# Performance work log

Hardware: AMD Instinct MI355X
Metric: run time of the kernel (lower is better)

The kernel has to match this reference:

```python
import jax, jax.numpy as jnp
import numpy as np

B, S, D = 4, 2048, 1024
H, DK, DV, DOUT = 16, 64, 64, 1024
NEG = -1.0e9


def setup_inputs() -> dict:
    key = jax.random.key(0)
    ks = jax.random.split(key, 12)
    sq = lambda fan_in: 1.0 / np.sqrt(fan_in)
    return {
        "query": jax.random.normal(ks[0], (B, S, D), jnp.float32),
        "key": jax.random.normal(ks[1], (B, S, D), jnp.float32),
        "value": jax.random.normal(ks[2], (B, S, D), jnp.float32),
        "attention_mask": jax.random.randint(ks[3], (B, 1, 1, S), 0, 2, jnp.int32),
        "wq": jax.random.normal(ks[4], (D, H * DK), jnp.float32) * sq(D),
        "bq": jnp.zeros((H * DK,), jnp.float32),
        "wk": jax.random.normal(ks[5], (D, H * DK), jnp.float32) * sq(D),
        "bk": jnp.zeros((H * DK,), jnp.float32),
        "wv": jax.random.normal(ks[6], (D, H * DV), jnp.float32) * sq(D),
        "bv": jnp.zeros((H * DV,), jnp.float32),
        "wo": jax.random.normal(ks[7], (H * DV, DOUT), jnp.float32) * sq(H * DV),
        "bo": jnp.zeros((DOUT,), jnp.float32),
    }


def _split_heads(x, head_dim):
    b, s, _ = x.shape
    return x.reshape(b, s, H, head_dim).transpose(0, 2, 1, 3)  # [B,H,S,hd]


def reference(query, key, value, attention_mask, wq, bq, wk, bk, wv, bv, wo, bo):
    q = _split_heads(query @ wq + bq, DK)   # [B,H,S,DK]
    k = _split_heads(key @ wk + bk, DK)     # [B,H,S,DK]
    v = _split_heads(value @ wv + bv, DV)   # [B,H,S,DV]
    logits = jnp.einsum("bhqd,bhkd->bhqk", q, k) / jnp.sqrt(jnp.float32(DK))
    logits = logits + attention_mask.astype(logits.dtype) * NEG
    attn = jax.nn.softmax(logits, axis=-1)
    out = jnp.einsum("bhqk,bhkd->bhqd", attn, v)          # [B,H,S,DV]
    out = out.transpose(0, 2, 1, 3).reshape(query.shape[0], -1, H * DV)
    return out @ wo + bo
```

## Files before the change

### kernel.cpp

```cpp
#include <hip/hip_runtime.h>
#include <hip/hip_bf16.h>
#include <math.h>

#define Bv 4
#define Sv 2048
#define Dv 1024
#define Hv 16
#define HD 64
#define NEGV (-1.0e9f)

typedef __attribute__((ext_vector_type(8))) short bf16x8;
typedef __attribute__((ext_vector_type(4))) short s16x4;
typedef __attribute__((ext_vector_type(4))) float f32x4;

__device__ __forceinline__ short f2bf(float f) {
    union { __hip_bfloat16 h; short s; } u;
    u.h = __float2bfloat16(f);
    return u.s;
}

#if __has_builtin(__builtin_amdgcn_exp2f)
#define EXP2F(x) __builtin_amdgcn_exp2f(x)
#else
#define EXP2F(x) __expf((x) * 0.6931471805599453f)
#endif

__device__ __forceinline__ void glds16(const void* g, void* l) {
    __builtin_amdgcn_global_load_lds(
        (const __attribute__((address_space(1))) void*)g,
        (__attribute__((address_space(3))) void*)l, 16, 0, 0);
}

__global__ __launch_bounds__(256) void cvt_bf16(const float* __restrict__ X,
                                                unsigned short* __restrict__ Y) {
    const size_t i = ((size_t)blockIdx.x * 256 + threadIdx.x) * 8;
    const float4 a = *(const float4*)&X[i];
    const float4 b = *(const float4*)&X[i + 4];
    bf16x8 o = {f2bf(a.x), f2bf(a.y), f2bf(a.z), f2bf(a.w),
                f2bf(b.x), f2bf(b.y), f2bf(b.z), f2bf(b.w)};
    *(bf16x8*)&Y[i] = o;
}

__device__ __forceinline__ void transpose_w_body(const float* __restrict__ W,
                                                 unsigned short* __restrict__ WT) {
    __shared__ float T[64][65];
    const int t = threadIdx.x;
    const int n0 = blockIdx.x * 64, k0 = blockIdx.y * 64;
    #pragma unroll
    for (int i = 0; i < 4; ++i) {
        const int k = (t >> 4) + 16 * i;
        const int nc = (t & 15) * 4;
        const float4 v = *(const float4*)&W[(size_t)(k0 + k) * 1024 + n0 + nc];
        T[k][nc + 0] = v.x; T[k][nc + 1] = v.y;
        T[k][nc + 2] = v.z; T[k][nc + 3] = v.w;
    }
    __syncthreads();
    const int n = t >> 2, kc = (t & 3) * 16;
    #pragma unroll
    for (int j4 = 0; j4 < 4; ++j4) {
        s16x4 o;
        #pragma unroll
        for (int jj = 0; jj < 4; ++jj) o[jj] = f2bf(T[kc + j4 * 4 + jj][n]);
        *(s16x4*)&WT[(size_t)(n0 + n) * 1024 + k0 + kc + j4 * 4] = o;
    }
}

__global__ __launch_bounds__(256) void transpose_w(const float* __restrict__ W,
                                                   unsigned short* __restrict__ WT) {
    transpose_w_body(W, WT);
}

__global__ __launch_bounds__(256) void transpose_w4(const float* __restrict__ W0,
                                                    const float* __restrict__ W1,
                                                    const float* __restrict__ W2,
                                                    const float* __restrict__ W3,
                                                    unsigned short* __restrict__ WTb) {
    const int z = blockIdx.z;
    const float* W = (z == 0) ? W0 : (z == 1) ? W1 : (z == 2) ? W2 : W3;
    transpose_w_body(W, WTb + (size_t)z * 1048576);
}

__global__ __launch_bounds__(256) void transpose_v(const unsigned short* __restrict__ Vin,
                                                   unsigned short* __restrict__ VT) {
    __shared__ unsigned short T[64][72];
    const int t = threadIdx.x;
    const int s0 = blockIdx.x * 64;
    const int bh = blockIdx.y;
    const size_t ib = (size_t)bh * Sv * 64;
    const size_t ob = (size_t)bh * 64 * Sv;
    {
        const int s = t >> 2, dc = (t & 3) * 16;
        const bf16x8 a = *(const bf16x8*)&Vin[ib + (size_t)(s0 + s) * 64 + dc];
        const bf16x8 b = *(const bf16x8*)&Vin[ib + (size_t)(s0 + s) * 64 + dc + 8];
        *(bf16x8*)&T[s][dc] = a;
        *(bf16x8*)&T[s][dc + 8] = b;
    }
    __syncthreads();
    const int dv = t >> 2, sc = (t & 3) * 16;
    #pragma unroll
    for (int j4 = 0; j4 < 4; ++j4) {
        s16x4 o;
        #pragma unroll
        for (int jj = 0; jj < 4; ++jj) o[jj] = (short)T[sc + j4 * 4 + jj][dv];
        *(s16x4*)&VT[ob + (size_t)dv * Sv + s0 + sc + j4 * 4] = o;
    }
}

template <int PERM>
__global__ __launch_bounds__(256) void gemm_mfma(const unsigned short* __restrict__ X,
                                                 const unsigned short* __restrict__ WT,
                                                 const float* __restrict__ bias,
                                                 void* __restrict__ Cv,
                                                 int M, int N, int K) {
    __shared__ short As[128 * 32];
    __shared__ short Bs[128 * 32];

    const int t = threadIdx.x;
    const int lane = t & 63, w = t >> 6;
    const int l15 = lane & 15, quad = lane >> 4;
    const int m0 = blockIdx.y * 128, n0 = blockIdx.x * 128;
    const int wm = (w >> 1) * 64, wn = (w & 1) * 64;

    f32x4 acc[4][4];
    #pragma unroll
    for (int mi = 0; mi < 4; ++mi)
        #pragma unroll
        for (int ni = 0; ni < 4; ++ni) acc[mi][ni] = (f32x4){0.f, 0.f, 0.f, 0.f};

    const int srow = lane >> 2;
    const int skc = (lane & 3) * 8;

    for (int k0 = 0; k0 < K; k0 += 32) {
        #pragma unroll
        for (int i = 0; i < 2; ++i) {
            const int seg = w * 2 + i;
            const int row = seg * 16 + srow;
            glds16(&WT[(size_t)(n0 + row) * K + k0 + skc], &Bs[seg * 512]);
            glds16(&X[(size_t)(m0 + row) * K + k0 + skc], &As[seg * 512]);
        }
        __syncthreads();

        bf16x8 afr[4], bfr[4];
        #pragma unroll
        for (int mi = 0; mi < 4; ++mi)
            afr[mi] = *(const bf16x8*)&As[(wm + mi * 16 + l15) * 32 + quad * 8];
        #pragma unroll
        for (int ni = 0; ni < 4; ++ni)
            bfr[ni] = *(const bf16x8*)&Bs[(wn + ni * 16 + l15) * 32 + quad * 8];
        #pragma unroll
        for (int mi = 0; mi < 4; ++mi)
            #pragma unroll
            for (int ni = 0; ni < 4; ++ni)
                acc[mi][ni] = __builtin_amdgcn_mfma_f32_16x16x32_bf16(
                    afr[mi], bfr[ni], acc[mi][ni], 0, 0, 0);
        __syncthreads();
    }

    #pragma unroll
    for (int mi = 0; mi < 4; ++mi) {
        #pragma unroll
        for (int ni = 0; ni < 4; ++ni) {
            const int col = n0 + wn + ni * 16 + l15;
            const float bsv = bias[col];
            #pragma unroll
            for (int r = 0; r < 4; ++r) {
                const int row = m0 + wm + mi * 16 + quad * 4 + r;
                const float vv = acc[mi][ni][r] + bsv;
                if constexpr (PERM == 0) {
                    ((float*)Cv)[(size_t)row * N + col] = vv;
                } else {
                    const int bb = row / Sv, s = row % Sv;
                    const int hh = col >> 6, d = col & 63;
                    ((unsigned short*)Cv)[((((size_t)bb * Hv + hh) * Sv + s) << 6) + d] =
                        (unsigned short)f2bf(vv);
                }
            }
        }
    }
}

__global__ __launch_bounds__(256) void gemm_qkv(const float* __restrict__ Xq,
                                                const float* __restrict__ Xk,
                                                const float* __restrict__ Xv,
                                                const unsigned short* __restrict__ WTb,
                                                const float* __restrict__ bq,
                                                const float* __restrict__ bk,
                                                const float* __restrict__ bv,
                                                unsigned short* __restrict__ Oq,
                                                unsigned short* __restrict__ Ok,
                                                unsigned short* __restrict__ Ov) {
    __shared__ short As[128 * 32];
    __shared__ short Bs[128 * 32];

    const int hw = blockIdx.x + 8 * (blockIdx.y + 64 * blockIdx.z);
    const int wl = (hw & 7) * 192 + (hw >> 3);
    const int bx = wl & 7, by = (wl >> 3) & 63, bz = wl >> 9;

    const float* X = (bz == 0) ? Xq : (bz == 1) ? Xk : Xv;
    const unsigned short* WT = WTb + (size_t)bz * 1048576;
    const float* bias = (bz == 0) ? bq : (bz == 1) ? bk : bv;

    const int t = threadIdx.x;
    const int lane = t & 63, w = t >> 6;
    const int l15 = lane & 15, quad = lane >> 4;
    const int m0 = by * 128, n0 = bx * 128;
    const int wm = (w >> 1) * 64, wn = (w & 1) * 64;

    f32x4 acc[4][4];
    #pragma unroll
    for (int mi = 0; mi < 4; ++mi)
        #pragma unroll
        for (int ni = 0; ni < 4; ++ni) acc[mi][ni] = (f32x4){0.f, 0.f, 0.f, 0.f};

    const int srow = lane >> 2;
    const int skc = (lane & 3) * 8;

    for (int k0 = 0; k0 < 1024; k0 += 32) {
        float4 fa[2][2];
        #pragma unroll
        for (int i = 0; i < 2; ++i) {
            const int seg = w * 2 + i;
            const int row = seg * 16 + srow;
            glds16(&WT[(size_t)(n0 + row) * 1024 + k0 + skc], &Bs[seg * 512]);
            const float* src = &X[(size_t)(m0 + row) * 1024 + k0 + skc];
            fa[i][0] = *(const float4*)src;
            fa[i][1] = *(const float4*)(src + 4);
        }
        #pragma unroll
        for (int i = 0; i < 2; ++i) {
            const int seg = w * 2 + i;
            bf16x8 o = {f2bf(fa[i][0].x), f2bf(fa[i][0].y), f2bf(fa[i][0].z), f2bf(fa[i][0].w),
                        f2bf(fa[i][1].x), f2bf(fa[i][1].y), f2bf(fa[i][1].z), f2bf(fa[i][1].w)};
            *(bf16x8*)&As[seg * 512 + lane * 8] = o;
        }
        __syncthreads();

        bf16x8 afr[4], bfr[4];
        #pragma unroll
        for (int mi = 0; mi < 4; ++mi)
            afr[mi] = *(const bf16x8*)&As[(wm + mi * 16 + l15) * 32 + quad * 8];
        #pragma unroll
        for (int ni = 0; ni < 4; ++ni)
            bfr[ni] = *(const bf16x8*)&Bs[(wn + ni * 16 + l15) * 32 + quad * 8];
        #pragma unroll
        for (int mi = 0; mi < 4; ++mi)
            #pragma unroll
            for (int ni = 0; ni < 4; ++ni)
                acc[mi][ni] = __builtin_amdgcn_mfma_f32_16x16x32_bf16(
                    afr[mi], bfr[ni], acc[mi][ni], 0, 0, 0);
        __syncthreads();
    }

    #pragma unroll
    for (int mi = 0; mi < 4; ++mi) {
        #pragma unroll
        for (int ni = 0; ni < 4; ++ni) {
            const int col = n0 + wn + ni * 16 + l15;
            const float bsv = bias[col];
            const int hh = col >> 6, d = col & 63;
            #pragma unroll
            for (int r = 0; r < 4; ++r) {
                const int row = m0 + wm + mi * 16 + quad * 4 + r;
                const int bb = row >> 11, s = row & 2047;
                const unsigned short v = (unsigned short)f2bf(acc[mi][ni][r] + bsv);
                if (bz == 2) {
                    Ov[((((size_t)bb * Hv + hh) * 64 + d) << 11) + s] = v;
                } else {
                    unsigned short* O = (bz == 0) ? Oq : Ok;
                    O[((((size_t)bb * Hv + hh) * Sv + s) << 6) + d] = v;
                }
            }
        }
    }
}

__global__ __launch_bounds__(256) void gemm_out(const unsigned short* __restrict__ Xp,
                                                const unsigned short* __restrict__ WT,
                                                const float* __restrict__ bias,
                                                float* __restrict__ C) {
    __shared__ short As[128 * 32];
    __shared__ short Bs[128 * 32];

    const int hw = blockIdx.x + 8 * blockIdx.y;
    const int wl = (hw & 7) * 64 + (hw >> 3);
    const int bx = wl & 7, by = wl >> 3;

    const int t = threadIdx.x;
    const int lane = t & 63, w = t >> 6;
    const int l15 = lane & 15, quad = lane >> 4;
    const int m0 = by * 128, n0 = bx * 128;
    const int wm = (w >> 1) * 64, wn = (w & 1) * 64;

    f32x4 acc[4][4];
    #pragma unroll
    for (int mi = 0; mi < 4; ++mi)
        #pragma unroll
        for (int ni = 0; ni < 4; ++ni) acc[mi][ni] = (f32x4){0.f, 0.f, 0.f, 0.f};

    const int srow = lane >> 2;
    const int skc = (lane & 3) * 8;

    for (int k0 = 0; k0 < 1024; k0 += 32) {
        const int hh = k0 >> 6, db = (k0 & 63);
        #pragma unroll
        for (int i = 0; i < 2; ++i) {
            const int seg = w * 2 + i;
            const int row = seg * 16 + srow;
            glds16(&WT[(size_t)(n0 + row) * 1024 + k0 + skc], &Bs[seg * 512]);
            const int rb = m0 + row;
            const int bb = rb >> 11, s = rb & 2047;
            glds16(&Xp[((((size_t)bb * Hv + hh) * Sv + s) << 6) + db + skc], &As[seg * 512]);
        }
        __syncthreads();

        bf16x8 afr[4], bfr[4];
        #pragma unroll
        for (int mi = 0; mi < 4; ++mi)
            afr[mi] = *(const bf16x8*)&As[(wm + mi * 16 + l15) * 32 + quad * 8];
        #pragma unroll
        for (int ni = 0; ni < 4; ++ni)
            bfr[ni] = *(const bf16x8*)&Bs[(wn + ni * 16 + l15) * 32 + quad * 8];
        #pragma unroll
        for (int mi = 0; mi < 4; ++mi)
            #pragma unroll
            for (int ni = 0; ni < 4; ++ni)
                acc[mi][ni] = __builtin_amdgcn_mfma_f32_16x16x32_bf16(
                    afr[mi], bfr[ni], acc[mi][ni], 0, 0, 0);
        __syncthreads();
    }

    #pragma unroll
    for (int mi = 0; mi < 4; ++mi) {
        #pragma unroll
        for (int ni = 0; ni < 4; ++ni) {
            const int col = n0 + wn + ni * 16 + l15;
            const float bsv = bias[col];
            #pragma unroll
            for (int r = 0; r < 4; ++r) {
                const int row = m0 + wm + mi * 16 + quad * 4 + r;
                C[(size_t)row * 1024 + col] = acc[mi][ni][r] + bsv;
            }
        }
    }
}

template <int OL>
__global__ __launch_bounds__(256, 4) void attn_mfma(const unsigned short* __restrict__ Q,
                                                    const unsigned short* __restrict__ Kg,
                                                    const unsigned short* __restrict__ VT,
                                                    const int* __restrict__ mask,
                                                    unsigned short* __restrict__ O) {
    __shared__ short Kl[64 * 72];
    __shared__ short Vl[64 * 72];
    __shared__ short Sl[128 * 72];
    __shared__ float Mk[64];

    const int t = threadIdx.x;
    const int lane = t & 63, w = t >> 6;
    const int l15 = lane & 15, quad = lane >> 4;
    const int q0 = blockIdx.x * 128;
    const int h = blockIdx.y, b = blockIdx.z;
    const int bh = b * Hv + h;
    const size_t kvb = (size_t)bh * Sv * 64;
    const size_t vtb = (size_t)bh * 64 * Sv;

    bf16x8 qf[2][2];
    #pragma unroll
    for (int ni = 0; ni < 2; ++ni) {
        const size_t qa = kvb + (size_t)(q0 + w * 32 + ni * 16 + l15) * 64 + quad * 8;
        qf[ni][0] = *(const bf16x8*)&Q[qa];
        qf[ni][1] = *(const bf16x8*)&Q[qa + 32];
    }

    float l_acc[2] = {0.f, 0.f};
    f32x4 oacc[2][4];
    #pragma unroll
    for (int mi = 0; mi < 2; ++mi)
        #pragma unroll
        for (int ni = 0; ni < 4; ++ni) oacc[mi][ni] = (f32x4){0.f, 0.f, 0.f, 0.f};

    const int srow = t >> 2, sch = (t & 3) * 16;
    const unsigned short* Kst = Kg + kvb + (size_t)srow * 64 + sch;
    const unsigned short* Vst = VT + vtb + (size_t)srow * Sv + sch;
    const int* Mst = mask + (size_t)b * Sv;

    bf16x8 kr0 = *(const bf16x8*)&Kst[0];
    bf16x8 kr1 = *(const bf16x8*)&Kst[8];
    bf16x8 vr0 = *(const bf16x8*)&Vst[0];
    bf16x8 vr1 = *(const bf16x8*)&Vst[8];
    int mreg = (t < 64) ? Mst[t] : 0;

    constexpr float CS = 0.18033688011112042f;
    constexpr float CM = NEGV * 1.4426950408889634f;

    for (int k0 = 0; k0 < Sv; k0 += 64) {
        __syncthreads();
        *(bf16x8*)&Kl[srow * 72 + sch] = kr0;
        *(bf16x8*)&Kl[srow * 72 + sch + 8] = kr1;
        *(bf16x8*)&Vl[srow * 72 + sch] = vr0;
        *(bf16x8*)&Vl[srow * 72 + sch + 8] = vr1;
        if (t < 64) Mk[t] = CM * (float)mreg;
        __syncthreads();

        if (k0 + 64 < Sv) {
            kr0 = *(const bf16x8*)&Kst[(size_t)(k0 + 64) * 64];
            kr1 = *(const bf16x8*)&Kst[(size_t)(k0 + 64) * 64 + 8];
            vr0 = *(const bf16x8*)&Vst[k0 + 64];
            vr1 = *(const bf16x8*)&Vst[k0 + 64 + 8];
            if (t < 64) mreg = Mst[k0 + 64 + t];
        }

        #pragma unroll
        for (int mi = 0; mi < 4; ++mi) {
            const bf16x8 kf0 = *(const bf16x8*)&Kl[(mi * 16 + l15) * 72 + quad * 8];
            const bf16x8 kf1 = *(const bf16x8*)&Kl[(mi * 16 + l15) * 72 + 32 + quad * 8];
            const float4 mk4 = *(const float4*)&Mk[mi * 16 + quad * 4];
            #pragma unroll
            for (int ni = 0; ni < 2; ++ni) {
                f32x4 st = (f32x4){0.f, 0.f, 0.f, 0.f};
                st = __builtin_amdgcn_mfma_f32_16x16x32_bf16(kf0, qf[ni][0], st, 0, 0, 0);
                st = __builtin_amdgcn_mfma_f32_16x16x32_bf16(kf1, qf[ni][1], st, 0, 0, 0);
                const float p0 = EXP2F(__builtin_fmaf(st[0], CS, mk4.x));
                const float p1 = EXP2F(__builtin_fmaf(st[1], CS, mk4.y));
                const float p2 = EXP2F(__builtin_fmaf(st[2], CS, mk4.z));
                const float p3 = EXP2F(__builtin_fmaf(st[3], CS, mk4.w));
                l_acc[ni] += (p0 + p1) + (p2 + p3);
                s16x4 pv = {f2bf(p0), f2bf(p1), f2bf(p2), f2bf(p3)};
                *(s16x4*)&Sl[(w * 32 + ni * 16 + l15) * 72 + mi * 16 + quad * 4] = pv;
            }
        }

        bf16x8 vf[4][2];
        #pragma unroll
        for (int ni = 0; ni < 4; ++ni) {
            vf[ni][0] = *(const bf16x8*)&Vl[(ni * 16 + l15) * 72 + quad * 8];
            vf[ni][1] = *(const bf16x8*)&Vl[(ni * 16 + l15) * 72 + 32 + quad * 8];
        }

        #pragma unroll
        for (int mi = 0; mi < 2; ++mi) {
            const bf16x8 pf0 = *(const bf16x8*)&Sl[(w * 32 + mi * 16 + l15) * 72 + quad * 8];
            const bf16x8 pf1 = *(const bf16x8*)&Sl[(w * 32 + mi * 16 + l15) * 72 + 32 + quad * 8];
            #pragma unroll
            for (int ni = 0; ni < 4; ++ni) {
                oacc[mi][ni] = __builtin_amdgcn_mfma_f32_16x16x32_bf16(pf0, vf[ni][0], oacc[mi][ni], 0, 0, 0);
                oacc[mi][ni] = __builtin_amdgcn_mfma_f32_16x16x32_bf16(pf1, vf[ni][1], oacc[mi][ni], 0, 0, 0);
            }
        }
    }

    #pragma unroll
    for (int mi = 0; mi < 2; ++mi) {
        float l = l_acc[mi];
        l += __shfl_xor(l, 16);
        l += __shfl_xor(l, 32);
        #pragma unroll
        for (int r = 0; r < 4; ++r) {
            const float lr = __shfl(l, quad * 4 + r, 64);
            const float inv = 1.0f / lr;
            const int s = q0 + w * 32 + mi * 16 + quad * 4 + r;
            #pragma unroll
            for (int ni = 0; ni < 4; ++ni) {
                const unsigned short v = (unsigned short)f2bf(oacc[mi][ni][r] * inv);
                if constexpr (OL == 0) {
                    O[((size_t)b * Sv + s) * (Hv * HD) + h * HD + ni * 16 + l15] = v;
                } else {
                    O[kvb + ((size_t)s << 6) + ni * 16 + l15] = v;
                }
            }
        }
    }
}

extern "C" void kernel_launch(void* const* d_in, const int* in_sizes, int n_in,
                              void* d_out, int out_size, void* d_ws, size_t ws_size,
                              hipStream_t stream) {
    const float* query = (const float*)d_in[0];
    const float* key   = (const float*)d_in[1];
    const float* value = (const float*)d_in[2];
    const int*   amask = (const int*)d_in[3];
    const float* wq = (const float*)d_in[4];
    const float* bq = (const float*)d_in[5];
    const float* wk = (const float*)d_in[6];
    const float* bk = (const float*)d_in[7];
    const float* wv = (const float*)d_in[8];
    const float* bv = (const float*)d_in[9];
    const float* wo = (const float*)d_in[10];
    const float* bo = (const float*)d_in[11];
    float* out = (float*)d_out;

    unsigned short* wsp = (unsigned short*)d_ws;
    dim3 bb(256);

    if (ws_size >= (size_t)64 * 1024 * 1024) {
        const size_t PBQ = (size_t)Bv * Hv * Sv * HD;
        unsigned short* qb = wsp;
        unsigned short* kb = qb + PBQ;
        unsigned short* vb = kb + PBQ;
        unsigned short* ab = vb + PBQ;

        transpose_w4<<<dim3(16, 16, 4), bb, 0, stream>>>(wq, wk, wv, wo, ab);

        gemm_qkv<<<dim3(8, 64, 3), bb, 0, stream>>>(query, key, value, ab,
                                                    bq, bk, bv, qb, kb, vb);

        attn_mfma<1><<<dim3(Sv / 128, Hv, Bv), bb, 0, stream>>>(qb, kb, vb, amask, qb);

        gemm_out<<<dim3(8, 64), bb, 0, stream>>>(qb, ab + (size_t)3 * 1048576, bo, out);
    } else {
        const size_t PQ = (size_t)Hv * Sv * HD;
        unsigned short* qb = wsp;
        unsigned short* kb = qb + PQ;
        unsigned short* vb = kb + PQ;
        unsigned short* ab = vb + PQ;
        const int M = Sv;
        dim3 gg(8, M / 128), gc(M * 1024 / 2048), gt(16, 16);
        for (int b = 0; b < Bv; ++b) {
            const size_t xoff = (size_t)b * Sv * Dv;
            unsigned short* wt_kb = kb;
            unsigned short* wt_out = (unsigned short*)(out + xoff);
            unsigned short* wt_vb = vb;

            cvt_bf16<<<gc, bb, 0, stream>>>(value + xoff, ab);
            transpose_w<<<gt, bb, 0, stream>>>(wv, wt_kb);
            gemm_mfma<1><<<gg, bb, 0, stream>>>(ab, wt_kb, bv, qb, M, 1024, 1024);
            transpose_v<<<dim3(Sv / 64, Hv), bb, 0, stream>>>(qb, vb);

            cvt_bf16<<<gc, bb, 0, stream>>>(query + xoff, ab);
            transpose_w<<<gt, bb, 0, stream>>>(wq, wt_kb);
            gemm_mfma<1><<<gg, bb, 0, stream>>>(ab, wt_kb, bq, qb, M, 1024, 1024);

            cvt_bf16<<<gc, bb, 0, stream>>>(key + xoff, ab);
            transpose_w<<<gt, bb, 0, stream>>>(wk, wt_out);
            gemm_mfma<1><<<gg, bb, 0, stream>>>(ab, wt_out, bk, kb, M, 1024, 1024);

            attn_mfma<0><<<dim3(Sv / 128, Hv, 1), bb, 0, stream>>>(qb, kb, vb,
                                                                   amask + (size_t)b * Sv, ab);

            transpose_w<<<gt, bb, 0, stream>>>(wo, wt_vb);
            gemm_mfma<0><<<gg, bb, 0, stream>>>(ab, wt_vb, bo, out + xoff, M, 1024, 1024);
        }
    }
}
```

Before: 394.3 us.

## Pre-convert QKV inputs to bf16 and load GEMM A tiles via global_load_lds

Adds a cvt3 kernel that converts query/key/value from fp32 to bf16 in a separate pass. The QKV projection GEMM then loads its A tiles directly into LDS with global_load_lds instead of loading fp32 into registers and converting in the inner loop. The aim is to cut register pressure and per-iteration conversion work and halve the A-operand bytes the GEMM reads. The cost is an extra kernel launch and an extra full write and read of the bf16 activations. When the workspace is mid-sized, the output buffer is borrowed as conversion scratch and the projection is split into two launches.

```diff
diff --git a/kernel.cpp b/kernel.cpp
--- a/kernel.cpp
+++ b/kernel.cpp
@@ -33,6 +33,23 @@
 
 __global__ __launch_bounds__(256) void cvt_bf16(const float* __restrict__ X,
                                                 unsigned short* __restrict__ Y) {
+    const size_t i = ((size_t)blockIdx.x * 256 + threadIdx.x) * 8;
+    const float4 a = *(const float4*)&X[i];
+    const float4 b = *(const float4*)&X[i + 4];
+    bf16x8 o = {f2bf(a.x), f2bf(a.y), f2bf(a.z), f2bf(a.w),
+                f2bf(b.x), f2bf(b.y), f2bf(b.z), f2bf(b.w)};
+    *(bf16x8*)&Y[i] = o;
+}
+
+__global__ __launch_bounds__(256) void cvt3(const float* __restrict__ x0,
+                                            const float* __restrict__ x1,
+                                            const float* __restrict__ x2,
+                                            unsigned short* __restrict__ y0,
+                                            unsigned short* __restrict__ y1,
+                                            unsigned short* __restrict__ y2) {
+    const int zz = blockIdx.y;
+    const float* X = (zz == 0) ? x0 : (zz == 1) ? x1 : x2;
+    unsigned short* Y = (zz == 0) ? y0 : (zz == 1) ? y1 : y2;
     const size_t i = ((size_t)blockIdx.x * 256 + threadIdx.x) * 8;
     const float4 a = *(const float4*)&X[i];
     const float4 b = *(const float4*)&X[i + 4];
@@ -179,26 +196,30 @@
     }
 }
 
-__global__ __launch_bounds__(256) void gemm_qkv(const float* __restrict__ Xq,
-                                                const float* __restrict__ Xk,
-                                                const float* __restrict__ Xv,
-                                                const unsigned short* __restrict__ WTb,
-                                                const float* __restrict__ bq,
-                                                const float* __restrict__ bk,
-                                                const float* __restrict__ bv,
-                                                unsigned short* __restrict__ Oq,
-                                                unsigned short* __restrict__ Ok,
-                                                unsigned short* __restrict__ Ov) {
+__global__ __launch_bounds__(256) void gemm_qkv_b(const unsigned short* __restrict__ Xq,
+                                                  const unsigned short* __restrict__ Xk,
+                                                  const unsigned short* __restrict__ Xv,
+                                                  const unsigned short* __restrict__ WTb,
+                                                  const float* __restrict__ bq,
+                                                  const float* __restrict__ bk,
+                                                  const float* __restrict__ bv,
+                                                  unsigned short* __restrict__ Oq,
+                                                  unsigned short* __restrict__ Ok,
+                                                  unsigned short* __restrict__ Ov,
+                                                  int za, int zb, int zc) {
     __shared__ short As[128 * 32];
     __shared__ short Bs[128 * 32];
 
+    const int nz = gridDim.z;
     const int hw = blockIdx.x + 8 * (blockIdx.y + 64 * blockIdx.z);
-    const int wl = (hw & 7) * 192 + (hw >> 3);
-    const int bx = wl & 7, by = (wl >> 3) & 63, bz = wl >> 9;
-
-    const float* X = (bz == 0) ? Xq : (bz == 1) ? Xk : Xv;
-    const unsigned short* WT = WTb + (size_t)bz * 1048576;
-    const float* bias = (bz == 0) ? bq : (bz == 1) ? bk : bv;
+    const int cpx = 64 * nz;
+    const int wl = (hw & 7) * cpx + (hw >> 3);
+    const int bx = wl & 7, by = (wl >> 3) & 63, bzr = wl >> 9;
+    const int z = (bzr == 0) ? za : (bzr == 1) ? zb : zc;
+
+    const unsigned short* X = (z == 0) ? Xq : (z == 1) ? Xk : Xv;
+    const unsigned short* WT = WTb + (size_t)z * 1048576;
+    const float* bias = (z == 0) ? bq : (z == 1) ? bk : bv;
 
     const int t = threadIdx.x;
     const int lane = t & 63, w = t >> 6;
@@ -216,22 +237,12 @@
     const int skc = (lane & 3) * 8;
 
     for (int k0 = 0; k0 < 1024; k0 += 32) {
-        float4 fa[2][2];
         #pragma unroll
         for (int i = 0; i < 2; ++i) {
             const int seg = w * 2 + i;
             const int row = seg * 16 + srow;
             glds16(&WT[(size_t)(n0 + row) * 1024 + k0 + skc], &Bs[seg * 512]);
-            const float* src = &X[(size_t)(m0 + row) * 1024 + k0 + skc];
-            fa[i][0] = *(const float4*)src;
-            fa[i][1] = *(const float4*)(src + 4);
-        }
-        #pragma unroll
-        for (int i = 0; i < 2; ++i) {
-            const int seg = w * 2 + i;
-            bf16x8 o = {f2bf(fa[i][0].x), f2bf(fa[i][0].y), f2bf(fa[i][0].z), f2bf(fa[i][0].w),
-                        f2bf(fa[i][1].x), f2bf(fa[i][1].y), f2bf(fa[i][1].z), f2bf(fa[i][1].w)};
-            *(bf16x8*)&As[seg * 512 + lane * 8] = o;
+            glds16(&X[(size_t)(m0 + row) * 1024 + k0 + skc], &As[seg * 512]);
         }
         __syncthreads();
 
@@ -263,11 +274,11 @@
                 const int row = m0 + wm + mi * 16 + quad * 4 + r;
                 const int bb = row >> 11, s = row & 2047;
                 const unsigned short v = (unsigned short)f2bf(acc[mi][ni][r] + bsv);
-                if (bz == 2) {
+                if (z == 2) {
                     Ov[((((size_t)bb * Hv + hh) * 64 + d) << 11) + s] = v;
                 } else {
-                    unsigned short* O = (bz == 0) ? Oq : Ok;
-                    O[((((size_t)bb * Hv + hh) * Sv + s) << 6) + d] = v;
+                    unsigned short* Od = (z == 0) ? Oq : Ok;
+                    Od[((((size_t)bb * Hv + hh) * Sv + s) << 6) + d] = v;
                 }
             }
         }
@@ -491,21 +502,41 @@
 
     unsigned short* wsp = (unsigned short*)d_ws;
     dim3 bb(256);
-
-    if (ws_size >= (size_t)64 * 1024 * 1024) {
-        const size_t PBQ = (size_t)Bv * Hv * Sv * HD;
+    const size_t PBQ = (size_t)Bv * Hv * Sv * HD;
+
+    if (ws_size >= (size_t)112 * 1024 * 1024) {
         unsigned short* qb = wsp;
         unsigned short* kb = qb + PBQ;
         unsigned short* vb = kb + PBQ;
         unsigned short* ab = vb + PBQ;
+        unsigned short* xb0 = ab + PBQ;
+        unsigned short* xb1 = xb0 + PBQ;
+        unsigned short* xb2 = xb1 + PBQ;
 
         transpose_w4<<<dim3(16, 16, 4), bb, 0, stream>>>(wq, wk, wv, wo, ab);
-
-        gemm_qkv<<<dim3(8, 64, 3), bb, 0, stream>>>(query, key, value, ab,
-                                                    bq, bk, bv, qb, kb, vb);
-
+        cvt3<<<dim3(4096, 3), bb, 0, stream>>>(query, key, value, xb0, xb1, xb2);
+        gemm_qkv_b<<<dim3(8, 64, 3), bb, 0, stream>>>(xb0, xb1, xb2, ab,
+                                                      bq, bk, bv, qb, kb, vb, 0, 1, 2);
         attn_mfma<1><<<dim3(Sv / 128, Hv, Bv), bb, 0, stream>>>(qb, kb, vb, amask, qb);
-
+        gemm_out<<<dim3(8, 64), bb, 0, stream>>>(qb, ab + (size_t)3 * 1048576, bo, out);
+    } else if (ws_size >= (size_t)64 * 1024 * 1024) {
+        unsigned short* qb = wsp;
+        unsigned short* kb = qb + PBQ;
+        unsigned short* vb = kb + PBQ;
+        unsigned short* ab = vb + PBQ;
+        unsigned short* dout_s = (unsigned short*)d_out;
+        unsigned short* xv = dout_s;
+        unsigned short* xq = dout_s + PBQ;
+        unsigned short* xk = dout_s;
+
+        transpose_w4<<<dim3(16, 16, 4), bb, 0, stream>>>(wq, wk, wv, wo, ab);
+        cvt3<<<dim3(4096, 2), bb, 0, stream>>>(value, query, query, xv, xq, xq);
+        gemm_qkv_b<<<dim3(8, 64, 2), bb, 0, stream>>>(xq, xq, xv, ab,
+                                                      bq, bk, bv, qb, kb, vb, 2, 0, 0);
+        cvt3<<<dim3(4096, 1), bb, 0, stream>>>(key, key, key, xk, xk, xk);
+        gemm_qkv_b<<<dim3(8, 64, 1), bb, 0, stream>>>(xk, xk, xk, ab,
+                                                      bq, bk, bv, qb, kb, vb, 1, 1, 1);
+        attn_mfma<1><<<dim3(Sv / 128, Hv, Bv), bb, 0, stream>>>(qb, kb, vb, amask, qb);
         gemm_out<<<dim3(8, 64), bb, 0, stream>>>(qb, ab + (size_t)3 * 1048576, bo, out);
     } else {
         const size_t PQ = (size_t)Hv * Sv * HD;
```

New measurement: 385.5 us. -2.2%, faster.
